# Performance work log

Measured on AMD Instinct MI355X. Metric: run time of the kernel, lower is better.

## Reference

```python
import jax, jax.numpy as jnp
import numpy as np

M_HEADS = 8   # n_heads
N_POINTS = 4  # n_points


def setup_inputs() -> dict:
    key = jax.random.key(0)
    ks = jax.random.split(key, 12)
    B, Lq, Lin, C = 2, 1024, 4096, 256
    M, P = M_HEADS, N_POINTS
    f32 = jnp.float32
    return {
        "query": jax.random.normal(ks[0], (B, Lq, C), f32),
        "query_points": jax.random.normal(ks[1], (B, Lq, 3), f32),
        "inp": jax.random.normal(ks[2], (B, Lin, C), f32),
        "input_points": jax.random.normal(ks[3], (B, Lin, 3), f32),
        # learned params (torch Linear convention: weight (out,in))
        "Wv": jax.random.normal(ks[4], (C, C), f32) * 0.02,
        "bv": jnp.zeros((C,), f32),
        "Ws": jax.random.normal(ks[5], (M * P * 3, C), f32) * 0.02,
        "bs": jnp.zeros((M * P * 3,), f32),
        "Wa": jax.random.normal(ks[6], (M * P, C), f32) * 0.02,
        "ba": jnp.zeros((M * P,), f32),
        "Wo": jax.random.normal(ks[7], (C, C), f32) * 0.02,
        "bo": jnp.zeros((C,), f32),
    }


def _deform_attn_forward(query, query_points, inp, input_points,
                         Wv, bv, Ws, bs, Wa, ba, Wo, bo):
    M, P = M_HEADS, N_POINTS
    B, Lq, C = query.shape
    Lin = inp.shape[1]
    D = C // M  # d_per_head

    # value projection -> (B, Lin, M, D)
    value = (inp @ Wv.T + bv).reshape(B, Lin, M, D)

    # sampling locations: query_points + learned offsets -> (B, Lq, M, P, 3)
    off = (query @ Ws.T + bs).reshape(B, Lq, M, P, 3)
    loc = query_points[:, :, None, None, :] + off

    # attention weights, softmax over sampling points -> (B, Lq, M, P)
    attw = jax.nn.softmax((query @ Wa.T + ba).reshape(B, Lq, M, P), axis=-1)

    # --- KNN (k=1): nearest value point for each sampling location ---
    s = loc.reshape(B, Lq * M * P, 3)
    s = jax.lax.stop_gradient(s)           # argmin indices are non-differentiable
    vpts = jax.lax.stop_gradient(input_points)
    # squared-distance argmin: |v|^2 - 2 s.v suffices (|s|^2 constant per row)
    d = jnp.sum(vpts * vpts, axis=-1)[:, None, :] \
        - 2.0 * jnp.einsum('bnc,blc->bnl', s, vpts)   # (B, N, Lin)
    idx = jnp.argmin(d, axis=-1)                       # (B, Lq*M*P)
    idx = idx.reshape(B, Lq, M, P).transpose(0, 2, 1, 3)  # (B, M, Lq, P)

    # gather per-head features: gathered[b,m,q,p,:] = value[b, idx, m, :]
    vhead = value.transpose(0, 2, 1, 3)                 # (B, M, Lin, D)
    g = jnp.take_along_axis(vhead, idx.reshape(B, M, Lq * P)[..., None], axis=2)
    g = g.reshape(B, M, Lq, P, D)

    # weighted sum over sampling points, merge heads -> (B, Lq, C)
    out = jnp.einsum('bmqpd,bmqp->bqmd', g, attw.transpose(0, 2, 1, 3))
    out = out.reshape(B, Lq, C)
    return out @ Wo.T + bo


def reference(query, query_points, inp, input_points,
              Wv, bv, Ws, bs, Wa, ba, Wo, bo):
    return _deform_attn_forward(query, query_points, inp, input_points,
                                Wv, bv, Ws, bs, Wa, ba, Wo, bo)
```

## Files before the change

kernel.cpp:

```cpp
#include <hip/hip_runtime.h>

#define B_   2
#define LQ   1024
#define LIN  4096
#define CH   256
#define MH   8
#define NP   4

#define NPTS      (B_ * LQ * MH * NP)
#define SLICES    16
#define SLICE_LEN (LIN / SLICES)
#define KNN_PPT   4
#define KNN_THREADS 256

__global__ __launch_bounds__(256)
void gemm_nt_bias(const float* __restrict__ A, const float* __restrict__ B,
                  const float* __restrict__ bias, float* __restrict__ C,
                  int M, int N, int K) {
    __shared__ float As[32][64];
    __shared__ float Bs[32][64];
    const int tid = threadIdx.x;
    const int bm  = blockIdx.x * 64;
    const int bn  = blockIdx.y * 64;
    const int tx  = tid & 15;
    const int ty  = tid >> 4;
    const int lr  = tid >> 2;
    const int lk  = (tid & 3) * 8;

    const float* Ap = A + (size_t)(bm + lr) * K + lk;
    const float* Bp = B + (size_t)(bn + lr) * K + lk;

    float4 a0 = *reinterpret_cast<const float4*>(Ap);
    float4 a1 = *reinterpret_cast<const float4*>(Ap + 4);
    float4 b0 = *reinterpret_cast<const float4*>(Bp);
    float4 b1 = *reinterpret_cast<const float4*>(Bp + 4);

    float acc[4][4] = {};
    for (int k0 = 0; k0 < K; k0 += 32) {
        __syncthreads();
        As[lk + 0][lr] = a0.x; As[lk + 1][lr] = a0.y;
        As[lk + 2][lr] = a0.z; As[lk + 3][lr] = a0.w;
        As[lk + 4][lr] = a1.x; As[lk + 5][lr] = a1.y;
        As[lk + 6][lr] = a1.z; As[lk + 7][lr] = a1.w;
        Bs[lk + 0][lr] = b0.x; Bs[lk + 1][lr] = b0.y;
        Bs[lk + 2][lr] = b0.z; Bs[lk + 3][lr] = b0.w;
        Bs[lk + 4][lr] = b1.x; Bs[lk + 5][lr] = b1.y;
        Bs[lk + 6][lr] = b1.z; Bs[lk + 7][lr] = b1.w;
        __syncthreads();
        if (k0 + 32 < K) {
            a0 = *reinterpret_cast<const float4*>(Ap + k0 + 32);
            a1 = *reinterpret_cast<const float4*>(Ap + k0 + 36);
            b0 = *reinterpret_cast<const float4*>(Bp + k0 + 32);
            b1 = *reinterpret_cast<const float4*>(Bp + k0 + 36);
        }
#pragma unroll
        for (int k = 0; k < 32; ++k) {
            float4 a = *reinterpret_cast<const float4*>(&As[k][ty << 2]);
            float4 b = *reinterpret_cast<const float4*>(&Bs[k][tx << 2]);
            float ar[4] = {a.x, a.y, a.z, a.w};
            float br[4] = {b.x, b.y, b.z, b.w};
#pragma unroll
            for (int i = 0; i < 4; ++i)
#pragma unroll
                for (int j = 0; j < 4; ++j)
                    acc[i][j] = fmaf(ar[i], br[j], acc[i][j]);
        }
    }
#pragma unroll
    for (int i = 0; i < 4; ++i) {
        const int row = bm + (ty << 2) + i;
        const int col = bn + (tx << 2);
        float4 c;
        c.x = acc[i][0] + bias[col + 0];
        c.y = acc[i][1] + bias[col + 1];
        c.z = acc[i][2] + bias[col + 2];
        c.w = acc[i][3] + bias[col + 3];
        *reinterpret_cast<float4*>(C + (size_t)row * N + col) = c;
    }
}

__global__ __launch_bounds__(256)
void gemm_s_fused(const float* __restrict__ query,
                  const float* __restrict__ Ws, const float* __restrict__ bs,
                  const float* __restrict__ Wa, const float* __restrict__ ba,
                  const float* __restrict__ qpts,
                  float* __restrict__ loc, float* __restrict__ attw) {
    __shared__ float As[16][64];
    __shared__ float Bs[16][128];
    __shared__ float Ss[64][132];
    const int tid = threadIdx.x;
    const int rowbase = blockIdx.x * 64;
    const int tx = tid & 15;
    const int ty = tid >> 4;

    const int lr  = tid >> 2;
    const int lka = (tid & 3) * 4;
    const float* Ap = query + (size_t)(rowbase + lr) * CH + lka;
    const int n   = tid >> 1;
    const int lkb = (tid & 1) * 8;
    const float* Wrow = ((n < 96) ? (Ws + (size_t)n * CH)
                                  : (Wa + (size_t)(n - 96) * CH)) + lkb;
    float bj[8];
#pragma unroll
    for (int j = 0; j < 8; ++j) {
        int col = tx * 8 + j;
        bj[j] = (col < 96) ? bs[col] : ba[col - 96];
    }

    float4 a0 = *reinterpret_cast<const float4*>(Ap);
    float4 b0 = *reinterpret_cast<const float4*>(Wrow);
    float4 b1 = *reinterpret_cast<const float4*>(Wrow + 4);

    float acc[4][8] = {};
    for (int k0 = 0; k0 < CH; k0 += 16) {
        __syncthreads();
        As[lka + 0][lr] = a0.x; As[lka + 1][lr] = a0.y;
        As[lka + 2][lr] = a0.z; As[lka + 3][lr] = a0.w;
        Bs[lkb + 0][n] = b0.x; Bs[lkb + 1][n] = b0.y;
        Bs[lkb + 2][n] = b0.z; Bs[lkb + 3][n] = b0.w;
        Bs[lkb + 4][n] = b1.x; Bs[lkb + 5][n] = b1.y;
        Bs[lkb + 6][n] = b1.z; Bs[lkb + 7][n] = b1.w;
        __syncthreads();
        if (k0 + 16 < CH) {
            a0 = *reinterpret_cast<const float4*>(Ap + k0 + 16);
            b0 = *reinterpret_cast<const float4*>(Wrow + k0 + 16);
            b1 = *reinterpret_cast<const float4*>(Wrow + k0 + 20);
        }
#pragma unroll
        for (int k = 0; k < 16; ++k) {
            float4 a  = *reinterpret_cast<const float4*>(&As[k][ty << 2]);
            float4 v0 = *reinterpret_cast<const float4*>(&Bs[k][tx * 8]);
            float4 v1 = *reinterpret_cast<const float4*>(&Bs[k][tx * 8 + 4]);
            float ar[4] = {a.x, a.y, a.z, a.w};
            float br[8] = {v0.x, v0.y, v0.z, v0.w, v1.x, v1.y, v1.z, v1.w};
#pragma unroll
            for (int i = 0; i < 4; ++i)
#pragma unroll
                for (int j = 0; j < 8; ++j)
                    acc[i][j] = fmaf(ar[i], br[j], acc[i][j]);
        }
    }

    __syncthreads();
#pragma unroll
    for (int i = 0; i < 4; ++i)
#pragma unroll
        for (int j = 0; j < 8; ++j)
            Ss[ty * 4 + i][tx * 8 + j] = acc[i][j] + bj[j];
    __syncthreads();

#pragma unroll
    for (int half = 0; half < 2; ++half) {
        int u   = tid + half * 256;
        int row = u >> 3;
        int m   = u & 7;
        int r   = rowbase + row;
        const float* Sr = Ss[row];
        float q0 = qpts[r * 3 + 0], q1 = qpts[r * 3 + 1], q2 = qpts[r * 3 + 2];
#pragma unroll
        for (int p = 0; p < NP; ++p) {
            size_t o = ((size_t)(r * MH + m) * NP + p) * 3;
            loc[o + 0] = q0 + Sr[m * 12 + p * 3 + 0];
            loc[o + 1] = q1 + Sr[m * 12 + p * 3 + 1];
            loc[o + 2] = q2 + Sr[m * 12 + p * 3 + 2];
        }
        float l0 = Sr[96 + m * 4 + 0], l1 = Sr[96 + m * 4 + 1];
        float l2 = Sr[96 + m * 4 + 2], l3 = Sr[96 + m * 4 + 3];
        float mx = fmaxf(fmaxf(l0, l1), fmaxf(l2, l3));
        float e0 = expf(l0 - mx), e1 = expf(l1 - mx);
        float e2 = expf(l2 - mx), e3 = expf(l3 - mx);
        float inv = 1.0f / (e0 + e1 + e2 + e3);
        size_t ao = (size_t)(r * MH + m) * NP;
        attw[ao + 0] = e0 * inv; attw[ao + 1] = e1 * inv;
        attw[ao + 2] = e2 * inv; attw[ao + 3] = e3 * inv;
    }
}

__global__ __launch_bounds__(KNN_THREADS)
void knn_partial_kernel(const float* __restrict__ loc, const float* __restrict__ ipts,
                        unsigned long long* __restrict__ keys) {
    __shared__ float4 pts[SLICE_LEN];
    const int slice = blockIdx.y;
    const int t0    = slice * SLICE_LEN;
    const int pt0   = blockIdx.x * (KNN_THREADS * KNN_PPT);
    const int b     = pt0 >> 15;

    {
        const float* sp = ipts + ((size_t)b * LIN + t0 + threadIdx.x) * 3;
        float x = sp[0], y = sp[1], z = sp[2];
        pts[threadIdx.x] = make_float4(x, y, z, fmaf(z, z, fmaf(y, y, x * x)));
    }

    float cx[KNN_PPT], cy[KNN_PPT], cz[KNN_PPT];
#pragma unroll
    for (int i = 0; i < KNN_PPT; ++i) {
        int p = pt0 + threadIdx.x + i * KNN_THREADS;
        cx[i] = -2.f * loc[(size_t)p * 3 + 0];
        cy[i] = -2.f * loc[(size_t)p * 3 + 1];
        cz[i] = -2.f * loc[(size_t)p * 3 + 2];
    }

    float bd[KNN_PPT][2];
    int   bi[KNN_PPT][2];
#pragma unroll
    for (int i = 0; i < KNN_PPT; ++i) {
        bd[i][0] = bd[i][1] = 1e30f;
        bi[i][0] = bi[i][1] = t0;
    }

    __syncthreads();
#pragma unroll 4
    for (int l = 0; l < SLICE_LEN; l += 2) {
        float4 p0 = pts[l + 0];
        float4 p1 = pts[l + 1];
#pragma unroll
        for (int i = 0; i < KNN_PPT; ++i) {
            float d0 = fmaf(cx[i], p0.x, fmaf(cy[i], p0.y, fmaf(cz[i], p0.z, p0.w)));
            float d1 = fmaf(cx[i], p1.x, fmaf(cy[i], p1.y, fmaf(cz[i], p1.z, p1.w)));
            if (d0 < bd[i][0]) { bd[i][0] = d0; bi[i][0] = t0 + l; }
            if (d1 < bd[i][1]) { bd[i][1] = d1; bi[i][1] = t0 + l + 1; }
        }
    }

#pragma unroll
    for (int i = 0; i < KNN_PPT; ++i) {
        float d = bd[i][0]; int ix = bi[i][0];
        if (bd[i][1] < d || (bd[i][1] == d && bi[i][1] < ix)) { d = bd[i][1]; ix = bi[i][1]; }
        unsigned int ub = __float_as_uint(d);
        unsigned int k32 = ub ^ (((unsigned int)((int)ub >> 31)) | 0x80000000u);
        unsigned long long key = ((unsigned long long)k32 << 32) | (unsigned int)ix;
        int p = pt0 + threadIdx.x + i * KNN_THREADS;
        atomicMin(&keys[p], key);
    }
}

__global__ __launch_bounds__(256)
void gather_kernel(const float* __restrict__ value, const float* __restrict__ attw,
                   const unsigned long long* __restrict__ keys,
                   float* __restrict__ out1) {
    int bq = blockIdx.x;
    int c  = threadIdx.x;
    int m  = c >> 5;
    int b  = bq >> 10;
    size_t base = ((size_t)bq * MH + m) * NP;
    const float* vb = value + (size_t)b * LIN * CH;
    float acc = 0.f;
#pragma unroll
    for (int p = 0; p < NP; ++p) {
        int   i = (int)(keys[base + p] & 0xFFFFFFFFull);
        float w = attw[base + p];
        acc = fmaf(w, vb[(size_t)i * CH + c], acc);
    }
    out1[(size_t)bq * CH + c] = acc;
}

extern "C" void kernel_launch(void* const* d_in, const int* in_sizes, int n_in,
                              void* d_out, int out_size, void* d_ws, size_t ws_size,
                              hipStream_t stream) {
    const float* query = (const float*)d_in[0];
    const float* qpts  = (const float*)d_in[1];
    const float* inp   = (const float*)d_in[2];
    const float* ipts  = (const float*)d_in[3];
    const float* Wv    = (const float*)d_in[4];
    const float* bv    = (const float*)d_in[5];
    const float* Ws    = (const float*)d_in[6];
    const float* bs    = (const float*)d_in[7];
    const float* Wa    = (const float*)d_in[8];
    const float* ba    = (const float*)d_in[9];
    const float* Wo    = (const float*)d_in[10];
    const float* bo    = (const float*)d_in[11];
    float* out = (float*)d_out;

    float* ws    = (float*)d_ws;
    float* value = ws;
    float* out1  = value + (size_t)B_ * LIN * CH;
    float* loc   = out1 + (size_t)B_ * LQ * CH;
    float* attw  = loc + (size_t)NPTS * 3;
    unsigned long long* keys =
        (unsigned long long*)(attw + (size_t)NPTS);

    hipMemsetAsync(keys, 0xFF, (size_t)NPTS * sizeof(unsigned long long), stream);
    gemm_nt_bias<<<dim3(128, 4), 256, 0, stream>>>(inp, Wv, bv, value, 8192, 256, 256);
    gemm_s_fused<<<32, 256, 0, stream>>>(query, Ws, bs, Wa, ba, qpts, loc, attw);
    knn_partial_kernel<<<dim3(NPTS / (KNN_THREADS * KNN_PPT), SLICES),
                         KNN_THREADS, 0, stream>>>(loc, ipts, keys);
    gather_kernel<<<B_ * LQ, 256, 0, stream>>>(value, attw, keys, out1);
    gemm_nt_bias<<<dim3(32, 4), 256, 0, stream>>>(out1, Wo, bo, out, 2048, 256, 256);
}
```

Measured before the change: 170.6 us.

## Blend raw inputs before value projection and drop full value GEMM

Reorders the computation so the attention-weighted gather runs on raw input rows and the per-head Wv projection is applied afterwards to the blended rows, with bv folded in later. This avoids projecting all 8192 input rows when only the 2048 blended query rows need it. The head-wise projection is split over K into two partials that the output GEMM sums while loading. The memset of the keys buffer is folded into the offset kernel, which removes one launch. The new shared-memory tiles use an XOR swizzle, and the extra partial buffer adds some global memory traffic.

```diff
diff --git a/kernel.cpp b/kernel.cpp
--- a/kernel.cpp
+++ b/kernel.cpp
@@ -6,85 +6,23 @@
 #define CH   256
 #define MH   8
 #define NP   4
-
-#define NPTS      (B_ * LQ * MH * NP)
+#define NROW (B_ * LQ)
+#define NPTS (NROW * MH * NP)
+
 #define SLICES    16
 #define SLICE_LEN (LIN / SLICES)
 #define KNN_PPT   4
 #define KNN_THREADS 256
 
-__global__ __launch_bounds__(256)
-void gemm_nt_bias(const float* __restrict__ A, const float* __restrict__ B,
-                  const float* __restrict__ bias, float* __restrict__ C,
-                  int M, int N, int K) {
-    __shared__ float As[32][64];
-    __shared__ float Bs[32][64];
-    const int tid = threadIdx.x;
-    const int bm  = blockIdx.x * 64;
-    const int bn  = blockIdx.y * 64;
-    const int tx  = tid & 15;
-    const int ty  = tid >> 4;
-    const int lr  = tid >> 2;
-    const int lk  = (tid & 3) * 8;
-
-    const float* Ap = A + (size_t)(bm + lr) * K + lk;
-    const float* Bp = B + (size_t)(bn + lr) * K + lk;
-
-    float4 a0 = *reinterpret_cast<const float4*>(Ap);
-    float4 a1 = *reinterpret_cast<const float4*>(Ap + 4);
-    float4 b0 = *reinterpret_cast<const float4*>(Bp);
-    float4 b1 = *reinterpret_cast<const float4*>(Bp + 4);
-
-    float acc[4][4] = {};
-    for (int k0 = 0; k0 < K; k0 += 32) {
-        __syncthreads();
-        As[lk + 0][lr] = a0.x; As[lk + 1][lr] = a0.y;
-        As[lk + 2][lr] = a0.z; As[lk + 3][lr] = a0.w;
-        As[lk + 4][lr] = a1.x; As[lk + 5][lr] = a1.y;
-        As[lk + 6][lr] = a1.z; As[lk + 7][lr] = a1.w;
-        Bs[lk + 0][lr] = b0.x; Bs[lk + 1][lr] = b0.y;
-        Bs[lk + 2][lr] = b0.z; Bs[lk + 3][lr] = b0.w;
-        Bs[lk + 4][lr] = b1.x; Bs[lk + 5][lr] = b1.y;
-        Bs[lk + 6][lr] = b1.z; Bs[lk + 7][lr] = b1.w;
-        __syncthreads();
-        if (k0 + 32 < K) {
-            a0 = *reinterpret_cast<const float4*>(Ap + k0 + 32);
-            a1 = *reinterpret_cast<const float4*>(Ap + k0 + 36);
-            b0 = *reinterpret_cast<const float4*>(Bp + k0 + 32);
-            b1 = *reinterpret_cast<const float4*>(Bp + k0 + 36);
-        }
-#pragma unroll
-        for (int k = 0; k < 32; ++k) {
-            float4 a = *reinterpret_cast<const float4*>(&As[k][ty << 2]);
-            float4 b = *reinterpret_cast<const float4*>(&Bs[k][tx << 2]);
-            float ar[4] = {a.x, a.y, a.z, a.w};
-            float br[4] = {b.x, b.y, b.z, b.w};
-#pragma unroll
-            for (int i = 0; i < 4; ++i)
-#pragma unroll
-                for (int j = 0; j < 4; ++j)
-                    acc[i][j] = fmaf(ar[i], br[j], acc[i][j]);
-        }
-    }
-#pragma unroll
-    for (int i = 0; i < 4; ++i) {
-        const int row = bm + (ty << 2) + i;
-        const int col = bn + (tx << 2);
-        float4 c;
-        c.x = acc[i][0] + bias[col + 0];
-        c.y = acc[i][1] + bias[col + 1];
-        c.z = acc[i][2] + bias[col + 2];
-        c.w = acc[i][3] + bias[col + 3];
-        *reinterpret_cast<float4*>(C + (size_t)row * N + col) = c;
-    }
-}
+#define SWZ(r) ((((r) >> 2) & 7) << 2)
 
 __global__ __launch_bounds__(256)
 void gemm_s_fused(const float* __restrict__ query,
                   const float* __restrict__ Ws, const float* __restrict__ bs,
                   const float* __restrict__ Wa, const float* __restrict__ ba,
                   const float* __restrict__ qpts,
-                  float* __restrict__ loc, float* __restrict__ attw) {
+                  float* __restrict__ loc, float* __restrict__ attw,
+                  unsigned long long* __restrict__ keys) {
     __shared__ float As[16][64];
     __shared__ float Bs[16][128];
     __shared__ float Ss[64][132];
@@ -173,6 +111,8 @@
         size_t ao = (size_t)(r * MH + m) * NP;
         attw[ao + 0] = e0 * inv; attw[ao + 1] = e1 * inv;
         attw[ao + 2] = e2 * inv; attw[ao + 3] = e3 * inv;
+        unsigned long long* kp = keys + ao;
+        kp[0] = kp[1] = kp[2] = kp[3] = 0xFFFFFFFFFFFFFFFFull;
     }
 }
 
@@ -226,7 +166,7 @@
     for (int i = 0; i < KNN_PPT; ++i) {
         float d = bd[i][0]; int ix = bi[i][0];
         if (bd[i][1] < d || (bd[i][1] == d && bi[i][1] < ix)) { d = bd[i][1]; ix = bi[i][1]; }
-        unsigned int ub = __float_as_uint(d);
+        unsigned int ub  = __float_as_uint(d);
         unsigned int k32 = ub ^ (((unsigned int)((int)ub >> 31)) | 0x80000000u);
         unsigned long long key = ((unsigned long long)k32 << 32) | (unsigned int)ix;
         int p = pt0 + threadIdx.x + i * KNN_THREADS;
@@ -235,23 +175,147 @@
 }
 
 __global__ __launch_bounds__(256)
-void gather_kernel(const float* __restrict__ value, const float* __restrict__ attw,
-                   const unsigned long long* __restrict__ keys,
-                   float* __restrict__ out1) {
-    int bq = blockIdx.x;
-    int c  = threadIdx.x;
-    int m  = c >> 5;
-    int b  = bq >> 10;
-    size_t base = ((size_t)bq * MH + m) * NP;
-    const float* vb = value + (size_t)b * LIN * CH;
-    float acc = 0.f;
-#pragma unroll
-    for (int p = 0; p < NP; ++p) {
-        int   i = (int)(keys[base + p] & 0xFFFFFFFFull);
-        float w = attw[base + p];
-        acc = fmaf(w, vb[(size_t)i * CH + c], acc);
-    }
-    out1[(size_t)bq * CH + c] = acc;
+void blend_gemm_kernel(const float* __restrict__ inp, const float* __restrict__ attw,
+                       const unsigned long long* __restrict__ keys,
+                       const float* __restrict__ Wv, float* __restrict__ part) {
+    __shared__ float Ab[128][132];
+    __shared__ float Bs[32][132];
+    __shared__ int   ids[128][4];
+    __shared__ float ats[128][4];
+    const int t  = threadIdx.x;
+    const int rb = blockIdx.x * 128;
+    const int m  = blockIdx.y;
+    const int ks = blockIdx.z;
+    const int k0 = ks * 128;
+
+    if (t < 128) {
+        size_t base = ((size_t)(rb + t) * MH + m) * NP;
+#pragma unroll
+        for (int p = 0; p < NP; ++p) {
+            ids[t][p] = (int)(keys[base + p] & 0xFFFFFFFFull);
+            ats[t][p] = attw[base + p];
+        }
+    }
+#pragma unroll
+    for (int pass = 0; pass < 4; ++pass) {
+        int u  = pass * 256 + t;
+        int nn = u >> 5;
+        int cg = (u & 31) * 4;
+        float4 w = *reinterpret_cast<const float4*>(Wv + (size_t)(m * 32 + nn) * CH + k0 + cg);
+        *reinterpret_cast<float4*>(&Bs[nn][cg ^ SWZ(nn)]) = w;
+    }
+    __syncthreads();
+
+#pragma unroll
+    for (int pass = 0; pass < 16; ++pass) {
+        int u   = pass * 256 + t;
+        int row = u >> 5;
+        int cg  = (u & 31) * 4;
+        int bq  = rb + row;
+        const float* ib = inp + ((size_t)(bq >> 10) * LIN) * CH + k0 + cg;
+        float4 a = {0.f, 0.f, 0.f, 0.f};
+#pragma unroll
+        for (int p = 0; p < NP; ++p) {
+            float4 v = *reinterpret_cast<const float4*>(ib + (size_t)ids[row][p] * CH);
+            float w = ats[row][p];
+            a.x = fmaf(w, v.x, a.x); a.y = fmaf(w, v.y, a.y);
+            a.z = fmaf(w, v.z, a.z); a.w = fmaf(w, v.w, a.w);
+        }
+        *reinterpret_cast<float4*>(&Ab[row][cg ^ SWZ(row)]) = a;
+    }
+    __syncthreads();
+
+    const int ty = t >> 3;
+    const int tx = t & 7;
+    const int sA = SWZ(ty * 4);
+    const int sB = SWZ(tx * 4);
+    float acc[4][4] = {};
+    for (int k = 0; k < 128; k += 4) {
+        float4 a[4], b[4];
+#pragma unroll
+        for (int i = 0; i < 4; ++i)
+            a[i] = *reinterpret_cast<const float4*>(&Ab[ty * 4 + i][k ^ sA]);
+#pragma unroll
+        for (int j = 0; j < 4; ++j)
+            b[j] = *reinterpret_cast<const float4*>(&Bs[tx * 4 + j][k ^ sB]);
+#pragma unroll
+        for (int i = 0; i < 4; ++i)
+#pragma unroll
+            for (int j = 0; j < 4; ++j)
+                acc[i][j] = fmaf(a[i].x, b[j].x, fmaf(a[i].y, b[j].y,
+                             fmaf(a[i].z, b[j].z, fmaf(a[i].w, b[j].w, acc[i][j]))));
+    }
+#pragma unroll
+    for (int i = 0; i < 4; ++i) {
+        int bq = rb + ty * 4 + i;
+        float4 c = {acc[i][0], acc[i][1], acc[i][2], acc[i][3]};
+        *reinterpret_cast<float4*>(part + ((size_t)ks * MH * NROW + (size_t)m * NROW + bq) * 32 + tx * 4) = c;
+    }
+}
+
+__global__ __launch_bounds__(256)
+void out_gemm_kernel(const float* __restrict__ part, const float* __restrict__ bv,
+                     const float* __restrict__ Wo, const float* __restrict__ bo,
+                     float* __restrict__ out) {
+    __shared__ float Ab[64][260];
+    __shared__ float Bs[32][260];
+    const int t  = threadIdx.x;
+    const int rb = blockIdx.x * 64;
+    const int nb = blockIdx.y * 32;
+
+#pragma unroll
+    for (int pass = 0; pass < 16; ++pass) {
+        int u   = pass * 256 + t;
+        int row = u >> 6;
+        int cg  = (u & 63) * 4;
+        int bq  = rb + row;
+        int mm  = cg >> 5, d = cg & 31;
+        size_t pi = ((size_t)mm * NROW + bq) * 32 + d;
+        float4 v0 = *reinterpret_cast<const float4*>(part + pi);
+        float4 v1 = *reinterpret_cast<const float4*>(part + (size_t)MH * NROW * 32 + pi);
+        float4 bb = *reinterpret_cast<const float4*>(bv + cg);
+        float4 a  = {v0.x + v1.x + bb.x, v0.y + v1.y + bb.y,
+                     v0.z + v1.z + bb.z, v0.w + v1.w + bb.w};
+        *reinterpret_cast<float4*>(&Ab[row][cg ^ SWZ(row)]) = a;
+    }
+#pragma unroll
+    for (int pass = 0; pass < 8; ++pass) {
+        int u  = pass * 256 + t;
+        int nn = u >> 6;
+        int cg = (u & 63) * 4;
+        float4 w = *reinterpret_cast<const float4*>(Wo + (size_t)(nb + nn) * CH + cg);
+        *reinterpret_cast<float4*>(&Bs[nn][cg ^ SWZ(nn)]) = w;
+    }
+    __syncthreads();
+
+    const int ty = t >> 3;
+    const int tx = t & 7;
+    const int sA = SWZ(ty * 2);
+    const int sB = SWZ(tx * 4);
+    float acc[2][4] = {};
+    for (int k = 0; k < 256; k += 4) {
+        float4 a[2], b[4];
+#pragma unroll
+        for (int i = 0; i < 2; ++i)
+            a[i] = *reinterpret_cast<const float4*>(&Ab[ty * 2 + i][k ^ sA]);
+#pragma unroll
+        for (int j = 0; j < 4; ++j)
+            b[j] = *reinterpret_cast<const float4*>(&Bs[tx * 4 + j][k ^ sB]);
+#pragma unroll
+        for (int i = 0; i < 2; ++i)
+#pragma unroll
+            for (int j = 0; j < 4; ++j)
+                acc[i][j] = fmaf(a[i].x, b[j].x, fmaf(a[i].y, b[j].y,
+                             fmaf(a[i].z, b[j].z, fmaf(a[i].w, b[j].w, acc[i][j]))));
+    }
+#pragma unroll
+    for (int i = 0; i < 2; ++i) {
+        int bq = rb + ty * 2 + i;
+        int n  = nb + tx * 4;
+        float4 c = {acc[i][0] + bo[n + 0], acc[i][1] + bo[n + 1],
+                    acc[i][2] + bo[n + 2], acc[i][3] + bo[n + 3]};
+        *reinterpret_cast<float4*>(out + (size_t)bq * CH + n) = c;
+    }
 }
 
 extern "C" void kernel_launch(void* const* d_in, const int* in_sizes, int n_in,
@@ -271,19 +335,19 @@
     const float* bo    = (const float*)d_in[11];
     float* out = (float*)d_out;
 
-    float* ws    = (float*)d_ws;
-    float* value = ws;
-    float* out1  = value + (size_t)B_ * LIN * CH;
-    float* loc   = out1 + (size_t)B_ * LQ * CH;
-    float* attw  = loc + (size_t)NPTS * 3;
+    float* ws   = (float*)d_ws;
+    float* loc  = ws;
+    float* attw = loc + (size_t)NPTS * 3;
     unsigned long long* keys =
         (unsigned long long*)(attw + (size_t)NPTS);
-
-    hipMemsetAsync(keys, 0xFF, (size_t)NPTS * sizeof(unsigned long long), stream);
-    gemm_nt_bias<<<dim3(128, 4), 256, 0, stream>>>(inp, Wv, bv, value, 8192, 256, 256);
-    gemm_s_fused<<<32, 256, 0, stream>>>(query, Ws, bs, Wa, ba, qpts, loc, attw);
+    float* part = (float*)(keys + (size_t)NPTS);
+
+    gemm_s_fused<<<NROW / 64, 256, 0, stream>>>(query, Ws, bs, Wa, ba, qpts,
+                                                loc, attw, keys);
     knn_partial_kernel<<<dim3(NPTS / (KNN_THREADS * KNN_PPT), SLICES),
                          KNN_THREADS, 0, stream>>>(loc, ipts, keys);
-    gather_kernel<<<B_ * LQ, 256, 0, stream>>>(value, attw, keys, out1);
-    gemm_nt_bias<<<dim3(32, 4), 256, 0, stream>>>(out1, Wo, bo, out, 2048, 256, 256);
-}
+    blend_gemm_kernel<<<dim3(NROW / 128, MH, 2), 256, 0, stream>>>(
+        inp, attw, keys, Wv, part);
+    out_gemm_kernel<<<dim3(NROW / 64, CH / 32), 256, 0, stream>>>(
+        part, bv, Wo, bo, out);
+}
```

New measurement: 160.7 us. -5.8%, faster.
